# Kernel optimization log

Hardware: AMD Instinct MI355X
Metric: run time of the kernel (lower is better)

The kernel has to match this reference:

```python
import jax, jax.numpy as jnp
import numpy as np

N_NODES = 100000
LEAKY_SLOPE = 0.01  # nn.LeakyReLU default

def setup_inputs() -> dict:
    key = jax.random.key(0)
    k1, k2, k3, k4, k5, k6 = jax.random.split(key, 6)
    in_dim, out_dim, ef_dim = 64, 64, 32
    E = 500000
    nf = jax.random.normal(k1, (N_NODES, in_dim), dtype=jnp.float32)
    ef = jax.random.normal(k2, (E, ef_dim), dtype=jnp.float32)
    src = jax.random.randint(k3, (E,), 0, N_NODES, dtype=jnp.int64 if jax.config.jax_enable_x64 else jnp.int32)
    dst = jax.random.randint(k4, (E,), 0, N_NODES, dtype=src.dtype)
    # torch Linear weights: (out, in), no bias
    We = jax.random.normal(k5, (out_dim, 2 * in_dim + ef_dim), dtype=jnp.float32) * 0.05
    Wn = jax.random.normal(k6, (out_dim, out_dim + in_dim), dtype=jnp.float32) * 0.05
    return {"nf": nf, "ef": ef, "src": src, "dst": dst, "We": We, "Wn": Wn}

def reference(nf, ef, src, dst, We, Wn):
    # Module adds reverse edges sharing the same edge features
    src_all = jnp.concatenate([src, dst])          # [2E]
    dst_all = jnp.concatenate([dst, src])          # [2E]
    ef_all = jnp.concatenate([ef, ef], axis=0)     # [2E, ef_dim]
    # message: concat(src_nf, dst_nf, ef) -> Linear -> LeakyReLU
    m_in = jnp.concatenate([nf[src_all], nf[dst_all], ef_all], axis=-1)  # [2E, 2*in+ef]
    msg = jax.nn.leaky_relu(m_in @ We.T, negative_slope=LEAKY_SLOPE)     # [2E, out]
    # reduce: sum messages at destination nodes
    red = jax.ops.segment_sum(msg, dst_all, num_segments=N_NODES)       # [N, out]
    # apply: concat(nf, red_msg) -> Linear -> LeakyReLU
    n_in = jnp.concatenate([nf, red], axis=-1)                          # [N, in+out]
    out_nf = jax.nn.leaky_relu(n_in @ Wn.T, negative_slope=LEAKY_SLOPE)
    return out_nf
```

## Files before the change

### kernel.cpp

```cpp
#include <hip/hip_runtime.h>
#include <stdint.h>


#define LEAKY(x) fmaxf((x), 0.01f * (x))
#define CAP 40
typedef _Float16 f16;
typedef _Float16 h2 __attribute__((ext_vector_type(2)));
typedef int iv4 __attribute__((ext_vector_type(4)));

static __device__ __forceinline__ int swz(int k, int c) {
    return k * 128 + (c ^ (((k >> 2) & 7) << 2));
}

union H4 { f16 h[4]; h2 p[2]; short4 s; long long ll; };
union H8 { f16 h[8]; h2 p[4]; int4 q; };

__global__ void prep_weights_kernel(const float* __restrict__ We,
                                    const float* __restrict__ Wn,
                                    float* __restrict__ WTab,
                                    float* __restrict__ WTc,
                                    float* __restrict__ WTn,
                                    int* __restrict__ cnt, int N)
{
    const int stride = gridDim.x * blockDim.x;
    int i = blockIdx.x * blockDim.x + threadIdx.x;
    for (int j = i; j < 8192 + 2048 + 8192; j += stride) {
        if (j < 8192) {
            int k = j >> 7, n = j & 127;
            WTab[j] = We[(n & 63) * 160 + (n >> 6) * 64 + k];
        } else if (j < 10240) {
            int q = j - 8192; int k = q >> 6, n = q & 63;
            WTc[q] = We[n * 160 + 128 + k];
        } else {
            int q = j - 10240; int k = q >> 6, n = q & 63;
            WTn[q] = Wn[n * 128 + k];
        }
    }
    const int C4 = N * 4;
    for (int j = i; j < C4; j += stride) cnt[j] = 0;
}

__global__ __launch_bounds__(256) void gemm_ab_kernel(
    const float4* __restrict__ nf4, const float* __restrict__ WT,
    f16* __restrict__ A16, f16* __restrict__ B16, int M)
{
    __shared__ float As[64 * 128];
    __shared__ float Ws[64 * 128];
    const int t = threadIdx.x;
    const int tr = t >> 4, tc = t & 15;
    const int m0 = blockIdx.x * 128;

    #pragma unroll
    for (int i = 0; i < 8; ++i)
        ((float4*)Ws)[t + 256 * i] = ((const float4*)WT)[t + 256 * i];
    #pragma unroll
    for (int i = 0; i < 8; ++i) {
        const int idx = t + 256 * i;
        const int m = idx >> 4, kq = idx & 15;
        float4 v = make_float4(0.f, 0.f, 0.f, 0.f);
        if (m0 + m < M) v = nf4[(size_t)(m0 + m) * 16 + kq];
        As[swz(4 * kq + 0, m)] = v.x;
        As[swz(4 * kq + 1, m)] = v.y;
        As[swz(4 * kq + 2, m)] = v.z;
        As[swz(4 * kq + 3, m)] = v.w;
    }
    __syncthreads();

    float acc[8][8];
    #pragma unroll
    for (int ri = 0; ri < 8; ++ri)
        #pragma unroll
        for (int ci = 0; ci < 8; ++ci) acc[ri][ci] = 0.f;

    #pragma unroll 8
    for (int k = 0; k < 64; ++k) {
        const float4 aLo = *(const float4*)&As[swz(k, tr * 4)];
        const float4 aHi = *(const float4*)&As[swz(k, 64 + tr * 4)];
        const float4 bLo = *(const float4*)&Ws[k * 128 + tc * 4];
        const float4 bHi = *(const float4*)&Ws[k * 128 + 64 + tc * 4];
        const float av[8] = {aLo.x, aLo.y, aLo.z, aLo.w, aHi.x, aHi.y, aHi.z, aHi.w};
        const float bv[8] = {bLo.x, bLo.y, bLo.z, bLo.w, bHi.x, bHi.y, bHi.z, bHi.w};
        #pragma unroll
        for (int ri = 0; ri < 8; ++ri)
            #pragma unroll
            for (int ci = 0; ci < 8; ++ci) acc[ri][ci] += av[ri] * bv[ci];
    }

    #pragma unroll
    for (int ri = 0; ri < 8; ++ri) {
        const int v = m0 + ((ri < 4) ? (tr * 4 + ri) : (64 + tr * 4 + ri - 4));
        if (v < M) {
            H4 lo, hi;
            #pragma unroll
            for (int j = 0; j < 4; ++j) { lo.h[j] = (f16)acc[ri][j]; hi.h[j] = (f16)acc[ri][4 + j]; }
            *(short4*)&A16[(size_t)v * 64 + tc * 4] = lo.s;
            *(short4*)&B16[(size_t)v * 64 + tc * 4] = hi.s;
        }
    }
}

__global__ __launch_bounds__(256) void gemm_p_kernel(
    const float4* __restrict__ nf4, const float* __restrict__ WTn,
    f16* __restrict__ P16, int M)
{
    __shared__ float As[64 * 128];
    __shared__ float Ws[64 * 64];
    const int t = threadIdx.x;
    const int tr = t >> 4, tc = t & 15;
    const int m0 = blockIdx.x * 128;

    #pragma unroll
    for (int i = 0; i < 4; ++i)
        ((float4*)Ws)[t + 256 * i] = ((const float4*)WTn)[t + 256 * i];
    #pragma unroll
    for (int i = 0; i < 8; ++i) {
        const int idx = t + 256 * i;
        const int m = idx >> 4, kq = idx & 15;
        float4 v = make_float4(0.f, 0.f, 0.f, 0.f);
        if (m0 + m < M) v = nf4[(size_t)(m0 + m) * 16 + kq];
        As[swz(4 * kq + 0, m)] = v.x;
        As[swz(4 * kq + 1, m)] = v.y;
        As[swz(4 * kq + 2, m)] = v.z;
        As[swz(4 * kq + 3, m)] = v.w;
    }
    __syncthreads();

    float acc[8][4];
    #pragma unroll
    for (int ri = 0; ri < 8; ++ri)
        #pragma unroll
        for (int ci = 0; ci < 4; ++ci) acc[ri][ci] = 0.f;

    #pragma unroll 8
    for (int k = 0; k < 64; ++k) {
        const float4 aLo = *(const float4*)&As[swz(k, tr * 4)];
        const float4 aHi = *(const float4*)&As[swz(k, 64 + tr * 4)];
        const float4 w  = *(const float4*)&Ws[k * 64 + tc * 4];
        const float av[8] = {aLo.x, aLo.y, aLo.z, aLo.w, aHi.x, aHi.y, aHi.z, aHi.w};
        const float bv[4] = {w.x, w.y, w.z, w.w};
        #pragma unroll
        for (int ri = 0; ri < 8; ++ri)
            #pragma unroll
            for (int ci = 0; ci < 4; ++ci) acc[ri][ci] += av[ri] * bv[ci];
    }

    #pragma unroll
    for (int ri = 0; ri < 8; ++ri) {
        const int v = m0 + ((ri < 4) ? (tr * 4 + ri) : (64 + tr * 4 + ri - 4));
        if (v < M) {
            H4 u;
            #pragma unroll
            for (int j = 0; j < 4; ++j) u.h[j] = (f16)acc[ri][j];
            *(short4*)&P16[(size_t)v * 64 + tc * 4] = u.s;
        }
    }
}

__global__ __launch_bounds__(256) void gemm_c_kernel(
    const float4* __restrict__ ef4, const float* __restrict__ WT,
    f16* __restrict__ C16, int M)
{
    __shared__ float As[32 * 128];
    __shared__ float Ws[32 * 64];
    const int t = threadIdx.x;
    const int tr = t >> 4, tc = t & 15;
    const int m0 = blockIdx.x * 128;

    #pragma unroll
    for (int i = 0; i < 2; ++i)
        ((float4*)Ws)[t + 256 * i] = ((const float4*)WT)[t + 256 * i];
    #pragma unroll
    for (int i = 0; i < 4; ++i) {
        const int idx = t + 256 * i;
        const int m = idx >> 3, kq = idx & 7;
        float4 v = make_float4(0.f, 0.f, 0.f, 0.f);
        if (m0 + m < M) v = ef4[(size_t)(m0 + m) * 8 + kq];
        As[swz(4 * kq + 0, m)] = v.x;
        As[swz(4 * kq + 1, m)] = v.y;
        As[swz(4 * kq + 2, m)] = v.z;
        As[swz(4 * kq + 3, m)] = v.w;
    }
    __syncthreads();

    float acc[8][4];
    #pragma unroll
    for (int ri = 0; ri < 8; ++ri)
        #pragma unroll
        for (int ci = 0; ci < 4; ++ci) acc[ri][ci] = 0.f;

    #pragma unroll 8
    for (int k = 0; k < 32; ++k) {
        const float4 aLo = *(const float4*)&As[swz(k, tr * 4)];
        const float4 aHi = *(const float4*)&As[swz(k, 64 + tr * 4)];
        const float4 w  = *(const float4*)&Ws[k * 64 + tc * 4];
        const float av[8] = {aLo.x, aLo.y, aLo.z, aLo.w, aHi.x, aHi.y, aHi.z, aHi.w};
        const float bv[4] = {w.x, w.y, w.z, w.w};
        #pragma unroll
        for (int ri = 0; ri < 8; ++ri)
            #pragma unroll
            for (int ci = 0; ci < 4; ++ci) acc[ri][ci] += av[ri] * bv[ci];
    }

    #pragma unroll
    for (int ri = 0; ri < 8; ++ri) {
        const int v = m0 + ((ri < 4) ? (tr * 4 + ri) : (64 + tr * 4 + ri - 4));
        if (v < M) {
            H4 u;
            #pragma unroll
            for (int j = 0; j < 4; ++j) u.h[j] = (f16)acc[ri][j];
            *(short4*)&C16[(size_t)v * 64 + tc * 4] = u.s;
        }
    }
}

__global__ __launch_bounds__(256) void scatter_kernel(
    const int* __restrict__ src, const int* __restrict__ dst,
    int* __restrict__ cnt, int2* __restrict__ inc, int E, int N)
{
    const int part = blockIdx.x & 7;
    const int lo = (int)(((long long)N * part) >> 3);
    const int hi = (int)(((long long)N * (part + 1)) >> 3);
    const int tid = (blockIdx.x >> 3) * blockDim.x + threadIdx.x;
    const int tpp = (gridDim.x >> 3) * blockDim.x;
    const int E4 = E >> 2;
    const iv4* src4 = (const iv4*)src;
    const iv4* dst4 = (const iv4*)dst;
    #define PUT(node, nbr, eid) \
        if ((node) >= plo && (node) < phi) { \
            const int p = atomicAdd(&cnt[(node) * 4], 1); \
            if (p < CAP) inc[(size_t)(node) * CAP + p] = make_int2((nbr) << 7, (eid) << 7); \
        }
    for (int ph = 0; ph < 2; ++ph) {
        const int plo = lo + (int)(((long long)(hi - lo) * ph) >> 1);
        const int phi = lo + (int)(((long long)(hi - lo) * (ph + 1)) >> 1);
        for (int j = tid; j < E4; j += tpp) {
            const iv4 s = __builtin_nontemporal_load(&src4[j]);
            const iv4 d = __builtin_nontemporal_load(&dst4[j]);
            const int e0 = 4 * j;
            PUT(d.x, s.x, e0 + 0)
            PUT(d.y, s.y, e0 + 1)
            PUT(d.z, s.z, e0 + 2)
            PUT(d.w, s.w, e0 + 3)
            PUT(s.x, d.x, e0 + 0)
            PUT(s.y, d.y, e0 + 1)
            PUT(s.z, d.z, e0 + 2)
            PUT(s.w, d.w, e0 + 3)
        }
        for (int i = (E4 << 2) + tid; i < E; i += tpp) {
            const int s = src[i], d = dst[i];
            PUT(d, s, i)
            PUT(s, d, i)
        }
    }
    #undef PUT
}

__global__ __launch_bounds__(256) void reduce_kernel(
    const f16* __restrict__ A16, const f16* __restrict__ B16,
    const f16* __restrict__ C16, const int* __restrict__ cnt,
    const int2* __restrict__ inc, f16* __restrict__ red16, int N)
{
    const int lane = threadIdx.x & 63;
    const int g = lane >> 3;
    const int sub = lane & 7;
    const int sub16 = sub * 16;
    const char* Ab = (const char*)A16;
    const char* Cb = (const char*)C16;
    const int part = blockIdx.x & 7;
    const int NO = (N + 7) >> 3;
    const int olo = (int)(((long long)NO * part) >> 3);
    const int ohi = (int)(((long long)NO * (part + 1)) >> 3);
    const int wid = (((blockIdx.x >> 3) * blockDim.x) + threadIdx.x) >> 6;
    const int wstride = ((gridDim.x >> 3) * blockDim.x) >> 6;
    const _Float16 k01 = (_Float16)0.01f;
    const h2 c001 = {k01, k01};
    for (int oct = olo + wid; oct < ohi; oct += wstride) {
        const int v = oct * 8 + g;
        const int vc = (v < N) ? v : (N - 1);
        const int len = min(cnt[vc * 4], CAP);
        const int ebase = vc * CAP;
        H8 bh; bh.q = *(const int4*)&B16[(size_t)vc * 64 + sub * 8];
        const h2 b0 = bh.p[0], b1 = bh.p[1], b2 = bh.p[2], b3 = bh.p[3];
        int mx = (len + 3) >> 2;
        mx = max(mx, __shfl_xor(mx, 8));
        mx = max(mx, __shfl_xor(mx, 16));
        mx = max(mx, __shfl_xor(mx, 32));
        float a0 = 0.f, a1 = 0.f, a2 = 0.f, a3 = 0.f;
        float a4 = 0.f, a5 = 0.f, a6 = 0.f, a7 = 0.f;
        for (int it = 0; it < mx; ++it) {
            const int el = it * 4;
            const int4 q0 = *(const int4*)&inc[ebase + el];
            const int4 q1 = *(const int4*)&inc[ebase + el + 2];
            float okf[4];
            unsigned ao[4], co[4];
            #pragma unroll
            for (int k2 = 0; k2 < 4; ++k2)
                okf[k2] = ((unsigned)(el + k2) < (unsigned)len) ? 1.0f : 0.0f;
            const int qa[4] = {q0.x, q0.z, q1.x, q1.z};
            const int qc[4] = {q0.y, q0.w, q1.y, q1.w};
            #pragma unroll
            for (int k2 = 0; k2 < 4; ++k2) {
                ao[k2] = (okf[k2] != 0.0f) ? (unsigned)qa[k2] : 0u;
                co[k2] = (okf[k2] != 0.0f) ? (unsigned)qc[k2] : 0u;
            }
            H8 Av[4], Cv[4];
            #pragma unroll
            for (int k2 = 0; k2 < 4; ++k2) {
                Av[k2].q = *(const int4*)(Ab + (size_t)ao[k2] + sub16);
                Cv[k2].q = *(const int4*)(Cb + (size_t)co[k2] + sub16);
            }
            #pragma unroll
            for (int k2 = 0; k2 < 4; ++k2) {
                h2 s0 = Av[k2].p[0] + Cv[k2].p[0] + b0;
                h2 s1 = Av[k2].p[1] + Cv[k2].p[1] + b1;
                h2 s2 = Av[k2].p[2] + Cv[k2].p[2] + b2;
                h2 s3 = Av[k2].p[3] + Cv[k2].p[3] + b3;
                s0 = __builtin_elementwise_max(s0, s0 * c001);
                s1 = __builtin_elementwise_max(s1, s1 * c001);
                s2 = __builtin_elementwise_max(s2, s2 * c001);
                s3 = __builtin_elementwise_max(s3, s3 * c001);
                a0 = fmaf((float)s0[0], okf[k2], a0);
                a1 = fmaf((float)s0[1], okf[k2], a1);
                a2 = fmaf((float)s1[0], okf[k2], a2);
                a3 = fmaf((float)s1[1], okf[k2], a3);
                a4 = fmaf((float)s2[0], okf[k2], a4);
                a5 = fmaf((float)s2[1], okf[k2], a5);
                a6 = fmaf((float)s3[0], okf[k2], a6);
                a7 = fmaf((float)s3[1], okf[k2], a7);
            }
        }
        if (v < N) {
            H8 u;
            u.h[0] = (f16)a0; u.h[1] = (f16)a1; u.h[2] = (f16)a2; u.h[3] = (f16)a3;
            u.h[4] = (f16)a4; u.h[5] = (f16)a5; u.h[6] = (f16)a6; u.h[7] = (f16)a7;
            *(int4*)&red16[(size_t)v * 64 + sub * 8] = u.q;
        }
    }
}

__global__ __launch_bounds__(256) void apply_lite_kernel(
    const f16* __restrict__ red16, const f16* __restrict__ P16,
    const float* __restrict__ WTn, float* __restrict__ out, int M)
{
    __shared__ float As[64 * 128];
    __shared__ float Ws[64 * 64];
    const int t = threadIdx.x;
    const int tr = t >> 4, tc = t & 15;
    const int m0 = blockIdx.x * 128;
    const float* WT1 = WTn + 4096;

    #pragma unroll
    for (int i = 0; i < 4; ++i)
        ((float4*)Ws)[t + 256 * i] = ((const float4*)WT1)[t + 256 * i];
    #pragma unroll
    for (int i = 0; i < 8; ++i) {
        const int idx = t + 256 * i;
        const int m = idx >> 4, kq = idx & 15;
        H4 v; v.ll = 0;
        if (m0 + m < M) v.s = *(const short4*)&red16[(size_t)(m0 + m) * 64 + kq * 4];
        As[swz(4 * kq + 0, m)] = (float)v.h[0];
        As[swz(4 * kq + 1, m)] = (float)v.h[1];
        As[swz(4 * kq + 2, m)] = (float)v.h[2];
        As[swz(4 * kq + 3, m)] = (float)v.h[3];
    }
    __syncthreads();

    float acc[8][4];
    #pragma unroll
    for (int ri = 0; ri < 8; ++ri)
        #pragma unroll
        for (int ci = 0; ci < 4; ++ci) acc[ri][ci] = 0.f;

    #pragma unroll 8
    for (int k = 0; k < 64; ++k) {
        const float4 aLo = *(const float4*)&As[swz(k, tr * 4)];
        const float4 aHi = *(const float4*)&As[swz(k, 64 + tr * 4)];
        const float4 w  = *(const float4*)&Ws[k * 64 + tc * 4];
        const float av[8] = {aLo.x, aLo.y, aLo.z, aLo.w, aHi.x, aHi.y, aHi.z, aHi.w};
        const float bv[4] = {w.x, w.y, w.z, w.w};
        #pragma unroll
        for (int ri = 0; ri < 8; ++ri)
            #pragma unroll
            for (int ci = 0; ci < 4; ++ci) acc[ri][ci] += av[ri] * bv[ci];
    }

    #pragma unroll
    for (int ri = 0; ri < 8; ++ri) {
        const int v = m0 + ((ri < 4) ? (tr * 4 + ri) : (64 + tr * 4 + ri - 4));
        if (v < M) {
            H4 pv; pv.s = *(const short4*)&P16[(size_t)v * 64 + tc * 4];
            float4 o;
            o.x = LEAKY(acc[ri][0] + (float)pv.h[0]);
            o.y = LEAKY(acc[ri][1] + (float)pv.h[1]);
            o.z = LEAKY(acc[ri][2] + (float)pv.h[2]);
            o.w = LEAKY(acc[ri][3] + (float)pv.h[3]);
            *(float4*)&out[(size_t)v * 64 + tc * 4] = o;
        }
    }
}

extern "C" void kernel_launch(void* const* d_in, const int* in_sizes, int n_in,
                              void* d_out, int out_size, void* d_ws, size_t ws_size,
                              hipStream_t stream) {
    const float* nf  = (const float*)d_in[0];
    const float* ef  = (const float*)d_in[1];
    const int*   src = (const int*)d_in[2];
    const int*   dst = (const int*)d_in[3];
    const float* We  = (const float*)d_in[4];
    const float* Wn  = (const float*)d_in[5];

    const int N = in_sizes[0] / 64;
    const int E = in_sizes[2];

    char* p = (char*)d_ws;
    auto alloc = [&](size_t bytes) -> char* {
        char* r = p; p += (bytes + 255) & ~(size_t)255; return r;
    };
    f16*   red16 = (f16*)alloc((size_t)N * 64 * 2);
    float* WTab  = (float*)alloc(8192 * 4);
    float* WTc   = (float*)alloc(2048 * 4);
    float* WTn   = (float*)alloc(8192 * 4);
    int2*  inc   = (int2*)alloc((size_t)N * CAP * 8);
    int*   cnt   = (int*)alloc((size_t)N * 4 * 4);
    f16*   A16   = (f16*)alloc((size_t)N * 64 * 2);
    f16*   B16   = (f16*)alloc((size_t)N * 64 * 2);
    f16*   C16   = (f16*)alloc((size_t)E * 64 * 2);
    f16*   P16   = (f16*)alloc((size_t)N * 64 * 2);

    const int NO = (N + 7) >> 3;
    const int redBlocks = (((NO + 3) / 4) + 7) & ~7;

    prep_weights_kernel<<<512, 256, 0, stream>>>(We, Wn, WTab, WTc, WTn, cnt, N);
    scatter_kernel<<<2048, 256, 0, stream>>>(src, dst, cnt, inc, E, N);
    gemm_c_kernel<<<(E + 127) / 128, 256, 0, stream>>>((const float4*)ef, WTc, C16, E);
    gemm_ab_kernel<<<(N + 127) / 128, 256, 0, stream>>>((const float4*)nf, WTab, A16, B16, N);
    gemm_p_kernel<<<(N + 127) / 128, 256, 0, stream>>>((const float4*)nf, WTn, P16, N);
    reduce_kernel<<<redBlocks, 256, 0, stream>>>(A16, B16, C16, cnt, inc, red16, N);
    apply_lite_kernel<<<(N + 127) / 128, 256, 0, stream>>>(red16, P16, WTn, (float*)d_out, N);
}
```

Before: 311.2 us.

## Merge scatter with edge GEMM, fuse node GEMMs, widen reduce gather loop

Scatter and the edge-feature GEMM now run in one launch, with block index deciding the role, so the two independent stages overlap. The A/B and P node GEMMs are fused into one kernel that loads each nf tile once. The scatter drops its two-phase node split. The reduce loop gathers 8 neighbors per iteration instead of 4 and gets a launch-bounds occupancy hint. This adds register pressure in the fused GEMM and the reduce, and may raise atomic contention in the scatter.

```diff
diff --git a/kernel.cpp b/kernel.cpp
--- a/kernel.cpp
+++ b/kernel.cpp
@@ -4,6 +4,7 @@
 
 #define LEAKY(x) fmaxf((x), 0.01f * (x))
 #define CAP 40
+#define SCAT_BLOCKS 2048
 typedef _Float16 f16;
 typedef _Float16 h2 __attribute__((ext_vector_type(2)));
 typedef int iv4 __attribute__((ext_vector_type(4)));
@@ -40,19 +41,131 @@
     for (int j = i; j < C4; j += stride) cnt[j] = 0;
 }
 
-__global__ __launch_bounds__(256) void gemm_ab_kernel(
-    const float4* __restrict__ nf4, const float* __restrict__ WT,
-    f16* __restrict__ A16, f16* __restrict__ B16, int M)
+static __device__ void scatter_body(int vb,
+    const int* __restrict__ src, const int* __restrict__ dst,
+    int* __restrict__ cnt, int2* __restrict__ inc, int E, int N)
+{
+    const int part = vb & 7;
+    const int lo = (int)(((long long)N * part) >> 3);
+    const int hi = (int)(((long long)N * (part + 1)) >> 3);
+    const int tid = (vb >> 3) * 256 + threadIdx.x;
+    const int tpp = (SCAT_BLOCKS >> 3) * 256;
+    const int E4 = E >> 2;
+    const iv4* src4 = (const iv4*)src;
+    const iv4* dst4 = (const iv4*)dst;
+    #define PUT(node, nbr, eid) \
+        if ((node) >= lo && (node) < hi) { \
+            const int p = atomicAdd(&cnt[(node) * 4], 1); \
+            if (p < CAP) inc[(size_t)(node) * CAP + p] = make_int2((nbr) << 7, (eid) << 7); \
+        }
+    for (int j = tid; j < E4; j += tpp) {
+        const iv4 s = __builtin_nontemporal_load(&src4[j]);
+        const iv4 d = __builtin_nontemporal_load(&dst4[j]);
+        const int e0 = 4 * j;
+        PUT(d.x, s.x, e0 + 0)
+        PUT(d.y, s.y, e0 + 1)
+        PUT(d.z, s.z, e0 + 2)
+        PUT(d.w, s.w, e0 + 3)
+        PUT(s.x, d.x, e0 + 0)
+        PUT(s.y, d.y, e0 + 1)
+        PUT(s.z, d.z, e0 + 2)
+        PUT(s.w, d.w, e0 + 3)
+    }
+    for (int i = (E4 << 2) + tid; i < E; i += tpp) {
+        const int s = src[i], d = dst[i];
+        PUT(d, s, i)
+        PUT(s, d, i)
+    }
+    #undef PUT
+}
+
+static __device__ void gemm_c_body(float* lds, int bid,
+    const float4* __restrict__ ef4, const float* __restrict__ WT,
+    f16* __restrict__ C16, int M)
+{
+    float* As = lds;
+    float* Ws = lds + 4096;
+    const int t = threadIdx.x;
+    const int tr = t >> 4, tc = t & 15;
+    const int m0 = bid * 128;
+
+    #pragma unroll
+    for (int i = 0; i < 2; ++i)
+        ((float4*)Ws)[t + 256 * i] = ((const float4*)WT)[t + 256 * i];
+    #pragma unroll
+    for (int i = 0; i < 4; ++i) {
+        const int idx = t + 256 * i;
+        const int m = idx >> 3, kq = idx & 7;
+        float4 v = make_float4(0.f, 0.f, 0.f, 0.f);
+        if (m0 + m < M) v = ef4[(size_t)(m0 + m) * 8 + kq];
+        As[swz(4 * kq + 0, m)] = v.x;
+        As[swz(4 * kq + 1, m)] = v.y;
+        As[swz(4 * kq + 2, m)] = v.z;
+        As[swz(4 * kq + 3, m)] = v.w;
+    }
+    __syncthreads();
+
+    float acc[8][4];
+    #pragma unroll
+    for (int ri = 0; ri < 8; ++ri)
+        #pragma unroll
+        for (int ci = 0; ci < 4; ++ci) acc[ri][ci] = 0.f;
+
+    #pragma unroll 8
+    for (int k = 0; k < 32; ++k) {
+        const float4 aLo = *(const float4*)&As[swz(k, tr * 4)];
+        const float4 aHi = *(const float4*)&As[swz(k, 64 + tr * 4)];
+        const float4 w  = *(const float4*)&Ws[k * 64 + tc * 4];
+        const float av[8] = {aLo.x, aLo.y, aLo.z, aLo.w, aHi.x, aHi.y, aHi.z, aHi.w};
+        const float bv[4] = {w.x, w.y, w.z, w.w};
+        #pragma unroll
+        for (int ri = 0; ri < 8; ++ri)
+            #pragma unroll
+            for (int ci = 0; ci < 4; ++ci) acc[ri][ci] += av[ri] * bv[ci];
+    }
+
+    #pragma unroll
+    for (int ri = 0; ri < 8; ++ri) {
+        const int v = m0 + ((ri < 4) ? (tr * 4 + ri) : (64 + tr * 4 + ri - 4));
+        if (v < M) {
+            H4 u;
+            #pragma unroll
+            for (int j = 0; j < 4; ++j) u.h[j] = (f16)acc[ri][j];
+            *(short4*)&C16[(size_t)v * 64 + tc * 4] = u.s;
+        }
+    }
+}
+
+__global__ __launch_bounds__(256) void mega1_kernel(
+    const int* __restrict__ src, const int* __restrict__ dst,
+    int* __restrict__ cnt, int2* __restrict__ inc,
+    const float4* __restrict__ ef4, const float* __restrict__ WTc,
+    f16* __restrict__ C16, int E, int N)
+{
+    __shared__ float lds[6144];
+    const int b = blockIdx.x;
+    if (b < SCAT_BLOCKS) scatter_body(b, src, dst, cnt, inc, E, N);
+    else                 gemm_c_body(lds, b - SCAT_BLOCKS, ef4, WTc, C16, E);
+}
+
+__global__ __launch_bounds__(256) void gemm_abp_kernel(
+    const float4* __restrict__ nf4, const float* __restrict__ WTab,
+    const float* __restrict__ WTn,
+    f16* __restrict__ A16, f16* __restrict__ B16, f16* __restrict__ P16, int M)
 {
     __shared__ float As[64 * 128];
-    __shared__ float Ws[64 * 128];
+    __shared__ float Wab[64 * 128];
+    __shared__ float Wp[64 * 64];
     const int t = threadIdx.x;
     const int tr = t >> 4, tc = t & 15;
     const int m0 = blockIdx.x * 128;
 
     #pragma unroll
     for (int i = 0; i < 8; ++i)
-        ((float4*)Ws)[t + 256 * i] = ((const float4*)WT)[t + 256 * i];
+        ((float4*)Wab)[t + 256 * i] = ((const float4*)WTab)[t + 256 * i];
+    #pragma unroll
+    for (int i = 0; i < 4; ++i)
+        ((float4*)Wp)[t + 256 * i] = ((const float4*)WTn)[t + 256 * i];
     #pragma unroll
     for (int i = 0; i < 8; ++i) {
         const int idx = t + 256 * i;
@@ -67,195 +180,53 @@
     __syncthreads();
 
     float acc[8][8];
-    #pragma unroll
-    for (int ri = 0; ri < 8; ++ri)
+    float accp[8][4];
+    #pragma unroll
+    for (int ri = 0; ri < 8; ++ri) {
         #pragma unroll
         for (int ci = 0; ci < 8; ++ci) acc[ri][ci] = 0.f;
-
-    #pragma unroll 8
+        #pragma unroll
+        for (int ci = 0; ci < 4; ++ci) accp[ri][ci] = 0.f;
+    }
+
+    #pragma unroll 4
     for (int k = 0; k < 64; ++k) {
         const float4 aLo = *(const float4*)&As[swz(k, tr * 4)];
         const float4 aHi = *(const float4*)&As[swz(k, 64 + tr * 4)];
-        const float4 bLo = *(const float4*)&Ws[k * 128 + tc * 4];
-        const float4 bHi = *(const float4*)&Ws[k * 128 + 64 + tc * 4];
+        const float4 bLo = *(const float4*)&Wab[k * 128 + tc * 4];
+        const float4 bHi = *(const float4*)&Wab[k * 128 + 64 + tc * 4];
+        const float4 w  = *(const float4*)&Wp[k * 64 + tc * 4];
         const float av[8] = {aLo.x, aLo.y, aLo.z, aLo.w, aHi.x, aHi.y, aHi.z, aHi.w};
         const float bv[8] = {bLo.x, bLo.y, bLo.z, bLo.w, bHi.x, bHi.y, bHi.z, bHi.w};
-        #pragma unroll
-        for (int ri = 0; ri < 8; ++ri)
+        const float wv[4] = {w.x, w.y, w.z, w.w};
+        #pragma unroll
+        for (int ri = 0; ri < 8; ++ri) {
             #pragma unroll
             for (int ci = 0; ci < 8; ++ci) acc[ri][ci] += av[ri] * bv[ci];
+            #pragma unroll
+            for (int ci = 0; ci < 4; ++ci) accp[ri][ci] += av[ri] * wv[ci];
+        }
     }
 
     #pragma unroll
     for (int ri = 0; ri < 8; ++ri) {
         const int v = m0 + ((ri < 4) ? (tr * 4 + ri) : (64 + tr * 4 + ri - 4));
         if (v < M) {
-            H4 lo, hi;
-            #pragma unroll
-            for (int j = 0; j < 4; ++j) { lo.h[j] = (f16)acc[ri][j]; hi.h[j] = (f16)acc[ri][4 + j]; }
+            H4 lo, hi, pu;
+            #pragma unroll
+            for (int j = 0; j < 4; ++j) {
+                lo.h[j] = (f16)acc[ri][j];
+                hi.h[j] = (f16)acc[ri][4 + j];
+                pu.h[j] = (f16)accp[ri][j];
+            }
             *(short4*)&A16[(size_t)v * 64 + tc * 4] = lo.s;
             *(short4*)&B16[(size_t)v * 64 + tc * 4] = hi.s;
-        }
-    }
-}
-
-__global__ __launch_bounds__(256) void gemm_p_kernel(
-    const float4* __restrict__ nf4, const float* __restrict__ WTn,
-    f16* __restrict__ P16, int M)
-{
-    __shared__ float As[64 * 128];
-    __shared__ float Ws[64 * 64];
-    const int t = threadIdx.x;
-    const int tr = t >> 4, tc = t & 15;
-    const int m0 = blockIdx.x * 128;
-
-    #pragma unroll
-    for (int i = 0; i < 4; ++i)
-        ((float4*)Ws)[t + 256 * i] = ((const float4*)WTn)[t + 256 * i];
-    #pragma unroll
-    for (int i = 0; i < 8; ++i) {
-        const int idx = t + 256 * i;
-        const int m = idx >> 4, kq = idx & 15;
-        float4 v = make_float4(0.f, 0.f, 0.f, 0.f);
-        if (m0 + m < M) v = nf4[(size_t)(m0 + m) * 16 + kq];
-        As[swz(4 * kq + 0, m)] = v.x;
-        As[swz(4 * kq + 1, m)] = v.y;
-        As[swz(4 * kq + 2, m)] = v.z;
-        As[swz(4 * kq + 3, m)] = v.w;
-    }
-    __syncthreads();
-
-    float acc[8][4];
-    #pragma unroll
-    for (int ri = 0; ri < 8; ++ri)
-        #pragma unroll
-        for (int ci = 0; ci < 4; ++ci) acc[ri][ci] = 0.f;
-
-    #pragma unroll 8
-    for (int k = 0; k < 64; ++k) {
-        const float4 aLo = *(const float4*)&As[swz(k, tr * 4)];
-        const float4 aHi = *(const float4*)&As[swz(k, 64 + tr * 4)];
-        const float4 w  = *(const float4*)&Ws[k * 64 + tc * 4];
-        const float av[8] = {aLo.x, aLo.y, aLo.z, aLo.w, aHi.x, aHi.y, aHi.z, aHi.w};
-        const float bv[4] = {w.x, w.y, w.z, w.w};
-        #pragma unroll
-        for (int ri = 0; ri < 8; ++ri)
-            #pragma unroll
-            for (int ci = 0; ci < 4; ++ci) acc[ri][ci] += av[ri] * bv[ci];
-    }
-
-    #pragma unroll
-    for (int ri = 0; ri < 8; ++ri) {
-        const int v = m0 + ((ri < 4) ? (tr * 4 + ri) : (64 + tr * 4 + ri - 4));
-        if (v < M) {
-            H4 u;
-            #pragma unroll
-            for (int j = 0; j < 4; ++j) u.h[j] = (f16)acc[ri][j];
-            *(short4*)&P16[(size_t)v * 64 + tc * 4] = u.s;
-        }
-    }
-}
-
-__global__ __launch_bounds__(256) void gemm_c_kernel(
-    const float4* __restrict__ ef4, const float* __restrict__ WT,
-    f16* __restrict__ C16, int M)
-{
-    __shared__ float As[32 * 128];
-    __shared__ float Ws[32 * 64];
-    const int t = threadIdx.x;
-    const int tr = t >> 4, tc = t & 15;
-    const int m0 = blockIdx.x * 128;
-
-    #pragma unroll
-    for (int i = 0; i < 2; ++i)
-        ((float4*)Ws)[t + 256 * i] = ((const float4*)WT)[t + 256 * i];
-    #pragma unroll
-    for (int i = 0; i < 4; ++i) {
-        const int idx = t + 256 * i;
-        const int m = idx >> 3, kq = idx & 7;
-        float4 v = make_float4(0.f, 0.f, 0.f, 0.f);
-        if (m0 + m < M) v = ef4[(size_t)(m0 + m) * 8 + kq];
-        As[swz(4 * kq + 0, m)] = v.x;
-        As[swz(4 * kq + 1, m)] = v.y;
-        As[swz(4 * kq + 2, m)] = v.z;
-        As[swz(4 * kq + 3, m)] = v.w;
-    }
-    __syncthreads();
-
-    float acc[8][4];
-    #pragma unroll
-    for (int ri = 0; ri < 8; ++ri)
-        #pragma unroll
-        for (int ci = 0; ci < 4; ++ci) acc[ri][ci] = 0.f;
-
-    #pragma unroll 8
-    for (int k = 0; k < 32; ++k) {
-        const float4 aLo = *(const float4*)&As[swz(k, tr * 4)];
-        const float4 aHi = *(const float4*)&As[swz(k, 64 + tr * 4)];
-        const float4 w  = *(const float4*)&Ws[k * 64 + tc * 4];
-        const float av[8] = {aLo.x, aLo.y, aLo.z, aLo.w, aHi.x, aHi.y, aHi.z, aHi.w};
-        const float bv[4] = {w.x, w.y, w.z, w.w};
-        #pragma unroll
-        for (int ri = 0; ri < 8; ++ri)
-            #pragma unroll
-            for (int ci = 0; ci < 4; ++ci) acc[ri][ci] += av[ri] * bv[ci];
-    }
-
-    #pragma unroll
-    for (int ri = 0; ri < 8; ++ri) {
-        const int v = m0 + ((ri < 4) ? (tr * 4 + ri) : (64 + tr * 4 + ri - 4));
-        if (v < M) {
-            H4 u;
-            #pragma unroll
-            for (int j = 0; j < 4; ++j) u.h[j] = (f16)acc[ri][j];
-            *(short4*)&C16[(size_t)v * 64 + tc * 4] = u.s;
-        }
-    }
-}
-
-__global__ __launch_bounds__(256) void scatter_kernel(
-    const int* __restrict__ src, const int* __restrict__ dst,
-    int* __restrict__ cnt, int2* __restrict__ inc, int E, int N)
-{
-    const int part = blockIdx.x & 7;
-    const int lo = (int)(((long long)N * part) >> 3);
-    const int hi = (int)(((long long)N * (part + 1)) >> 3);
-    const int tid = (blockIdx.x >> 3) * blockDim.x + threadIdx.x;
-    const int tpp = (gridDim.x >> 3) * blockDim.x;
-    const int E4 = E >> 2;
-    const iv4* src4 = (const iv4*)src;
-    const iv4* dst4 = (const iv4*)dst;
-    #define PUT(node, nbr, eid) \
-        if ((node) >= plo && (node) < phi) { \
-            const int p = atomicAdd(&cnt[(node) * 4], 1); \
-            if (p < CAP) inc[(size_t)(node) * CAP + p] = make_int2((nbr) << 7, (eid) << 7); \
-        }
-    for (int ph = 0; ph < 2; ++ph) {
-        const int plo = lo + (int)(((long long)(hi - lo) * ph) >> 1);
-        const int phi = lo + (int)(((long long)(hi - lo) * (ph + 1)) >> 1);
-        for (int j = tid; j < E4; j += tpp) {
-            const iv4 s = __builtin_nontemporal_load(&src4[j]);
-            const iv4 d = __builtin_nontemporal_load(&dst4[j]);
-            const int e0 = 4 * j;
-            PUT(d.x, s.x, e0 + 0)
-            PUT(d.y, s.y, e0 + 1)
-            PUT(d.z, s.z, e0 + 2)
-            PUT(d.w, s.w, e0 + 3)
-            PUT(s.x, d.x, e0 + 0)
-            PUT(s.y, d.y, e0 + 1)
-            PUT(s.z, d.z, e0 + 2)
-            PUT(s.w, d.w, e0 + 3)
-        }
-        for (int i = (E4 << 2) + tid; i < E; i += tpp) {
-            const int s = src[i], d = dst[i];
-            PUT(d, s, i)
-            PUT(s, d, i)
-        }
-    }
-    #undef PUT
-}
-
-__global__ __launch_bounds__(256) void reduce_kernel(
+            *(short4*)&P16[(size_t)v * 64 + tc * 4] = pu.s;
+        }
+    }
+}
+
+__global__ __launch_bounds__(256, 4) void reduce_kernel(
     const f16* __restrict__ A16, const f16* __restrict__ B16,
     const f16* __restrict__ C16, const int* __restrict__ cnt,
     const int2* __restrict__ inc, f16* __restrict__ red16, int N)
@@ -281,36 +252,38 @@
         const int ebase = vc * CAP;
         H8 bh; bh.q = *(const int4*)&B16[(size_t)vc * 64 + sub * 8];
         const h2 b0 = bh.p[0], b1 = bh.p[1], b2 = bh.p[2], b3 = bh.p[3];
-        int mx = (len + 3) >> 2;
+        int mx = (len + 7) >> 3;
         mx = max(mx, __shfl_xor(mx, 8));
         mx = max(mx, __shfl_xor(mx, 16));
         mx = max(mx, __shfl_xor(mx, 32));
         float a0 = 0.f, a1 = 0.f, a2 = 0.f, a3 = 0.f;
         float a4 = 0.f, a5 = 0.f, a6 = 0.f, a7 = 0.f;
         for (int it = 0; it < mx; ++it) {
-            const int el = it * 4;
+            const int el = it * 8;
             const int4 q0 = *(const int4*)&inc[ebase + el];
             const int4 q1 = *(const int4*)&inc[ebase + el + 2];
-            float okf[4];
-            unsigned ao[4], co[4];
-            #pragma unroll
-            for (int k2 = 0; k2 < 4; ++k2)
+            const int4 q2 = *(const int4*)&inc[ebase + el + 4];
+            const int4 q3 = *(const int4*)&inc[ebase + el + 6];
+            float okf[8];
+            unsigned ao[8], co[8];
+            #pragma unroll
+            for (int k2 = 0; k2 < 8; ++k2)
                 okf[k2] = ((unsigned)(el + k2) < (unsigned)len) ? 1.0f : 0.0f;
-            const int qa[4] = {q0.x, q0.z, q1.x, q1.z};
-            const int qc[4] = {q0.y, q0.w, q1.y, q1.w};
-            #pragma unroll
-            for (int k2 = 0; k2 < 4; ++k2) {
+            const int qa[8] = {q0.x, q0.z, q1.x, q1.z, q2.x, q2.z, q3.x, q3.z};
+            const int qc[8] = {q0.y, q0.w, q1.y, q1.w, q2.y, q2.w, q3.y, q3.w};
+            #pragma unroll
+            for (int k2 = 0; k2 < 8; ++k2) {
                 ao[k2] = (okf[k2] != 0.0f) ? (unsigned)qa[k2] : 0u;
                 co[k2] = (okf[k2] != 0.0f) ? (unsigned)qc[k2] : 0u;
             }
-            H8 Av[4], Cv[4];
-            #pragma unroll
-            for (int k2 = 0; k2 < 4; ++k2) {
+            H8 Av[8], Cv[8];
+            #pragma unroll
+            for (int k2 = 0; k2 < 8; ++k2) {
                 Av[k2].q = *(const int4*)(Ab + (size_t)ao[k2] + sub16);
                 Cv[k2].q = *(const int4*)(Cb + (size_t)co[k2] + sub16);
             }
             #pragma unroll
-            for (int k2 = 0; k2 < 4; ++k2) {
+            for (int k2 = 0; k2 < 8; ++k2) {
                 h2 s0 = Av[k2].p[0] + Cv[k2].p[0] + b0;
                 h2 s1 = Av[k2].p[1] + Cv[k2].p[1] + b1;
                 h2 s2 = Av[k2].p[2] + Cv[k2].p[2] + b2;
@@ -427,14 +400,16 @@
     f16*   C16   = (f16*)alloc((size_t)E * 64 * 2);
     f16*   P16   = (f16*)alloc((size_t)N * 64 * 2);
 
+    const int nC = (E + 127) >> 7;
+    const int nAB = (N + 127) >> 7;
     const int NO = (N + 7) >> 3;
     const int redBlocks = (((NO + 3) / 4) + 7) & ~7;
 
     prep_weights_kernel<<<512, 256, 0, stream>>>(We, Wn, WTab, WTc, WTn, cnt, N);
-    scatter_kernel<<<2048, 256, 0, stream>>>(src, dst, cnt, inc, E, N);
-    gemm_c_kernel<<<(E + 127) / 128, 256, 0, stream>>>((const float4*)ef, WTc, C16, E);
-    gemm_ab_kernel<<<(N + 127) / 128, 256, 0, stream>>>((const float4*)nf, WTab, A16, B16, N);
-    gemm_p_kernel<<<(N + 127) / 128, 256, 0, stream>>>((const float4*)nf, WTn, P16, N);
+    mega1_kernel<<<SCAT_BLOCKS + nC, 256, 0, stream>>>(src, dst, cnt, inc,
+                                                       (const float4*)ef, WTc, C16, E, N);
+    gemm_abp_kernel<<<nAB, 256, 0, stream>>>((const float4*)nf, WTab, WTn,
+                                             A16, B16, P16, N);
     reduce_kernel<<<redBlocks, 256, 0, stream>>>(A16, B16, C16, cnt, inc, red16, N);
     apply_lite_kernel<<<(N + 127) / 128, 256, 0, stream>>>(red16, P16, WTn, (float*)d_out, N);
 }
```

Result: faster. 288.6 us (-7.2%).
